# Kernel optimization log

Measured on AMD Instinct MI355X. Metric: run time of the kernel, lower is better.

## Reference

```python
import jax, jax.numpy as jnp
import numpy as np

SHORT_RANGE_CUTOFF = 1.6
N_PAIRS = 20_000_000
N_ATOMS = 100_000


def setup_inputs() -> dict:
    key = jax.random.key(0)
    k1, k2, k3 = jax.random.split(key, 3)
    Rij = jax.random.normal(k1, (N_PAIRS, 3), dtype=jnp.float32)
    idx_i = jax.random.randint(k2, (N_PAIRS,), 0, N_ATOMS, dtype=jnp.int64)
    idx_j = jax.random.randint(k3, (N_PAIRS,), 0, N_ATOMS, dtype=jnp.int64)
    return {"Rij": Rij, "idx_i": idx_i, "idx_j": idx_j}


def reference(Rij, idx_i, idx_j):
    """Faithful jax version of FilterShortRange.forward.

    torch.nonzero produces a dynamic-size index set; under jit we express the
    same compaction as a fixed-size stable partition: all pairs with
    ||Rij|| <= cutoff are packed to the front (original relative order
    preserved, matching torch.nonzero's ascending-index order), the tail is
    padded (Rij rows zeroed, idx entries set to -1), and n_valid reports the
    true compacted length.
    """
    rij = jnp.linalg.norm(Rij, axis=-1)                 # [P]
    mask = rij <= SHORT_RANGE_CUTOFF                    # [P] bool
    # stable argsort of ~mask: valid (False=0) entries first, order preserved
    order = jnp.argsort(jnp.logical_not(mask), stable=True)  # [P]
    mask_sorted = mask[order]                           # [P]
    Rij_sr = jnp.where(mask_sorted[:, None], Rij[order], 0.0)
    idx_i_sr = jnp.where(mask_sorted, idx_i[order], -1)
    idx_j_sr = jnp.where(mask_sorted, idx_j[order], -1)
    n_valid = jnp.sum(mask.astype(jnp.int32))
    # long-range copies are the untouched originals
    return (Rij_sr, idx_i_sr, idx_j_sr, Rij, idx_i, idx_j, n_valid)
```

## Files before the change

kernel.cpp:

```cpp
#include <hip/hip_runtime.h>
#include <math.h>


#define BLOCK 256
#define VPT 4
#define CHUNK (BLOCK * VPT)
#define SCAN_T 1024

__device__ __forceinline__ bool short_mask(float x, float y, float z) {
    float s = x * x + y * y + z * z;
    return sqrtf(s) <= 1.6f;
}

__global__ __launch_bounds__(BLOCK) void count_kernel(
    const float* __restrict__ Rij, int* __restrict__ counts, int P) {
    int b = blockIdx.x;
    int tid = threadIdx.x;
    int e0 = b * CHUNK + tid * VPT;
    int cnt = 0;
    if ((e0 + VPT <= P) && ((P & 3) == 0)) {
        const float4* R4 = (const float4*)Rij + (e0 * 3) / 4;
        float4 a = R4[0], c = R4[1], d = R4[2];
        cnt += short_mask(a.x, a.y, a.z);
        cnt += short_mask(a.w, c.x, c.y);
        cnt += short_mask(c.z, c.w, d.x);
        cnt += short_mask(d.y, d.z, d.w);
    } else {
        for (int j = 0; j < VPT; ++j) {
            int p = e0 + j;
            if (p < P) {
                float x = Rij[3 * p], y = Rij[3 * p + 1], z = Rij[3 * p + 2];
                cnt += short_mask(x, y, z);
            }
        }
    }
    for (int off = 32; off > 0; off >>= 1) cnt += __shfl_down(cnt, off);
    __shared__ int sm[BLOCK / 64];
    int lane = tid & 63, wid = tid >> 6;
    if (lane == 0) sm[wid] = cnt;
    __syncthreads();
    if (tid == 0) {
        int t = 0;
        for (int w = 0; w < BLOCK / 64; ++w) t += sm[w];
        counts[b] = t;
    }
}

__global__ __launch_bounds__(SCAN_T) void scan_kernel(
    const int* __restrict__ counts, int* __restrict__ offsets, int nb,
    int* __restrict__ nvalid_ws, float* __restrict__ nvalid_out) {
    __shared__ int sm[SCAN_T];
    __shared__ int carry_s;
    int tid = threadIdx.x;
    if (tid == 0) carry_s = 0;
    __syncthreads();
    for (int start = 0; start < nb; start += SCAN_T) {
        int i = start + tid;
        int v = (i < nb) ? counts[i] : 0;
        sm[tid] = v;
        __syncthreads();
        for (int off = 1; off < SCAN_T; off <<= 1) {
            int y = (tid >= off) ? sm[tid - off] : 0;
            __syncthreads();
            sm[tid] += y;
            __syncthreads();
        }
        int incl = sm[tid];
        int carry = carry_s;
        if (i < nb) offsets[i] = carry + incl - v;
        __syncthreads();
        if (tid == 0) carry_s = carry + sm[SCAN_T - 1];
        __syncthreads();
    }
    if (tid == 0) {
        nvalid_ws[0] = carry_s;
        nvalid_out[0] = (float)carry_s;
    }
}

__global__ __launch_bounds__(BLOCK) void scatter_kernel(
    const float* __restrict__ Rij, const int* __restrict__ idx_i,
    const int* __restrict__ idx_j, const int* __restrict__ offsets,
    const int* __restrict__ nvalid_ws, float* __restrict__ out, int P) {
    int b = blockIdx.x;
    int tid = threadIdx.x;
    int lane = tid & 63, wid = tid >> 6;
    int e0 = b * CHUNK + tid * VPT;
    int nvalid = nvalid_ws[0];

    float x[VPT], y[VPT], z[VPT];
    int ii[VPT], jj[VPT];
    bool m[VPT], inr[VPT];

    bool fullvec = (e0 + VPT <= P) && ((P & 3) == 0);
    if (fullvec) {
        const float4* R4 = (const float4*)Rij + (e0 * 3) / 4;
        float4 a = R4[0], c = R4[1], d = R4[2];
        x[0] = a.x; y[0] = a.y; z[0] = a.z;
        x[1] = a.w; y[1] = c.x; z[1] = c.y;
        x[2] = c.z; y[2] = c.w; z[2] = d.x;
        x[3] = d.y; y[3] = d.z; z[3] = d.w;
        int4 vi = *((const int4*)idx_i + e0 / 4);
        int4 vj = *((const int4*)idx_j + e0 / 4);
        ii[0] = vi.x; ii[1] = vi.y; ii[2] = vi.z; ii[3] = vi.w;
        jj[0] = vj.x; jj[1] = vj.y; jj[2] = vj.z; jj[3] = vj.w;
        for (int j = 0; j < VPT; ++j) {
            inr[j] = true;
            m[j] = short_mask(x[j], y[j], z[j]);
        }
        float4* lrR = (float4*)(out + 5LL * P) + (e0 * 3) / 4;
        lrR[0] = a; lrR[1] = c; lrR[2] = d;
        float4 fi = make_float4((float)ii[0], (float)ii[1], (float)ii[2], (float)ii[3]);
        float4 fj = make_float4((float)jj[0], (float)jj[1], (float)jj[2], (float)jj[3]);
        *((float4*)(out + 8LL * P) + e0 / 4) = fi;
        *((float4*)(out + 9LL * P) + e0 / 4) = fj;
    } else {
        for (int j = 0; j < VPT; ++j) {
            int p = e0 + j;
            inr[j] = (p < P);
            if (inr[j]) {
                x[j] = Rij[3 * p]; y[j] = Rij[3 * p + 1]; z[j] = Rij[3 * p + 2];
                ii[j] = idx_i[p]; jj[j] = idx_j[p];
                m[j] = short_mask(x[j], y[j], z[j]);
                out[5LL * P + 3 * p] = x[j];
                out[5LL * P + 3 * p + 1] = y[j];
                out[5LL * P + 3 * p + 2] = z[j];
                out[8LL * P + p] = (float)ii[j];
                out[9LL * P + p] = (float)jj[j];
            } else {
                m[j] = false;
            }
        }
    }

    int cnt = 0;
    for (int j = 0; j < VPT; ++j) cnt += (inr[j] && m[j]);

    int xs = cnt;
    for (int off = 1; off < 64; off <<= 1) {
        int yv = __shfl_up(xs, off);
        if (lane >= off) xs += yv;
    }
    int waveExcl = xs - cnt;
    __shared__ int wsum[BLOCK / 64];
    if (lane == 63) wsum[wid] = xs;
    __syncthreads();
    int wpre = 0;
    for (int w = 0; w < wid; ++w) wpre += wsum[w];

    int base = offsets[b] + wpre + waveExcl;
    int thrPre = 0;
    for (int j = 0; j < VPT; ++j) {
        if (!inr[j]) continue;
        int p = e0 + j;
        int v = base + thrPre;
        if (m[j]) {
            out[3 * v] = x[j];
            out[3 * v + 1] = y[j];
            out[3 * v + 2] = z[j];
            out[3LL * P + v] = (float)ii[j];
            out[4LL * P + v] = (float)jj[j];
            ++thrPre;
        } else {
            int dst = nvalid + (p - v);
            out[3 * dst] = 0.0f;
            out[3 * dst + 1] = 0.0f;
            out[3 * dst + 2] = 0.0f;
            out[3LL * P + dst] = -1.0f;
            out[4LL * P + dst] = -1.0f;
        }
    }
}

extern "C" void kernel_launch(void* const* d_in, const int* in_sizes, int n_in,
                              void* d_out, int out_size, void* d_ws, size_t ws_size,
                              hipStream_t stream) {
    const float* Rij = (const float*)d_in[0];
    const int* idx_i = (const int*)d_in[1];
    const int* idx_j = (const int*)d_in[2];
    int P = in_sizes[1];
    float* out = (float*)d_out;

    int nb = (P + CHUNK - 1) / CHUNK;
    int* counts = (int*)d_ws;
    int* offsets = counts + nb;
    int* nvalid_ws = offsets + nb;

    count_kernel<<<nb, BLOCK, 0, stream>>>(Rij, counts, P);
    scan_kernel<<<1, SCAN_T, 0, stream>>>(counts, offsets, nb, nvalid_ws,
                                          out + 10LL * P);
    scatter_kernel<<<nb, BLOCK, 0, stream>>>(Rij, idx_i, idx_j, offsets,
                                             nvalid_ws, out, P);
}
```

Baseline: 1.153 ms.

## Stage compacted pairs in LDS for coalesced writes, parallelize scan, use nontemporal stores

```diff
diff --git a/kernel.cpp b/kernel.cpp
--- a/kernel.cpp
+++ b/kernel.cpp
@@ -6,6 +6,9 @@
 #define VPT 4
 #define CHUNK (BLOCK * VPT)
 #define SCAN_T 1024
+
+typedef float vf4 __attribute__((ext_vector_type(4)));
+typedef int vi4 __attribute__((ext_vector_type(4)));
 
 __device__ __forceinline__ bool short_mask(float x, float y, float z) {
     float s = x * x + y * y + z * z;
@@ -18,9 +21,9 @@
     int tid = threadIdx.x;
     int e0 = b * CHUNK + tid * VPT;
     int cnt = 0;
-    if ((e0 + VPT <= P) && ((P & 3) == 0)) {
-        const float4* R4 = (const float4*)Rij + (e0 * 3) / 4;
-        float4 a = R4[0], c = R4[1], d = R4[2];
+    if (e0 + VPT <= P) {
+        const vf4* R4 = (const vf4*)Rij + (e0 * 3) / 4;
+        vf4 a = R4[0], c = R4[1], d = R4[2];
         cnt += short_mask(a.x, a.y, a.z);
         cnt += short_mask(a.w, c.x, c.y);
         cnt += short_mask(c.z, c.w, d.x);
@@ -49,32 +52,38 @@
 __global__ __launch_bounds__(SCAN_T) void scan_kernel(
     const int* __restrict__ counts, int* __restrict__ offsets, int nb,
     int* __restrict__ nvalid_ws, float* __restrict__ nvalid_out) {
-    __shared__ int sm[SCAN_T];
-    __shared__ int carry_s;
     int tid = threadIdx.x;
-    if (tid == 0) carry_s = 0;
-    __syncthreads();
-    for (int start = 0; start < nb; start += SCAN_T) {
-        int i = start + tid;
-        int v = (i < nb) ? counts[i] : 0;
-        sm[tid] = v;
-        __syncthreads();
-        for (int off = 1; off < SCAN_T; off <<= 1) {
-            int y = (tid >= off) ? sm[tid - off] : 0;
-            __syncthreads();
-            sm[tid] += y;
-            __syncthreads();
-        }
-        int incl = sm[tid];
-        int carry = carry_s;
-        if (i < nb) offsets[i] = carry + incl - v;
-        __syncthreads();
-        if (tid == 0) carry_s = carry + sm[SCAN_T - 1];
-        __syncthreads();
+    int seg = (nb + SCAN_T - 1) / SCAN_T;
+    int s0 = tid * seg;
+    int local = 0;
+    for (int k = 0; k < seg; ++k) {
+        int i = s0 + k;
+        if (i < nb) local += counts[i];
+    }
+    int lane = tid & 63, wid = tid >> 6;
+    int incl = local;
+    for (int off = 1; off < 64; off <<= 1) {
+        int y = __shfl_up(incl, off);
+        if (lane >= off) incl += y;
+    }
+    __shared__ int wsum[SCAN_T / 64];
+    if (lane == 63) wsum[wid] = incl;
+    __syncthreads();
+    int wpre = 0;
+    for (int w = 0; w < wid; ++w) wpre += wsum[w];
+    int run = wpre + incl - local;
+    for (int k = 0; k < seg; ++k) {
+        int i = s0 + k;
+        if (i < nb) {
+            offsets[i] = run;
+            run += counts[i];
+        }
     }
     if (tid == 0) {
-        nvalid_ws[0] = carry_s;
-        nvalid_out[0] = (float)carry_s;
+        int tot = 0;
+        for (int w = 0; w < SCAN_T / 64; ++w) tot += wsum[w];
+        nvalid_ws[0] = tot;
+        nvalid_out[0] = (float)tot;
     }
 }
 
@@ -82,43 +91,44 @@
     const float* __restrict__ Rij, const int* __restrict__ idx_i,
     const int* __restrict__ idx_j, const int* __restrict__ offsets,
     const int* __restrict__ nvalid_ws, float* __restrict__ out, int P) {
+    __shared__ float rs[3 * CHUNK];
+    __shared__ int iis[CHUNK];
+    __shared__ int jjs[CHUNK];
+    __shared__ int wsums[BLOCK / 64];
+
     int b = blockIdx.x;
     int tid = threadIdx.x;
     int lane = tid & 63, wid = tid >> 6;
     int e0 = b * CHUNK + tid * VPT;
-    int nvalid = nvalid_ws[0];
 
     float x[VPT], y[VPT], z[VPT];
     int ii[VPT], jj[VPT];
-    bool m[VPT], inr[VPT];
-
-    bool fullvec = (e0 + VPT <= P) && ((P & 3) == 0);
-    if (fullvec) {
-        const float4* R4 = (const float4*)Rij + (e0 * 3) / 4;
-        float4 a = R4[0], c = R4[1], d = R4[2];
+    bool m[VPT];
+
+    if (e0 + VPT <= P) {
+        const vf4* R4 = (const vf4*)Rij + (e0 * 3) / 4;
+        vf4 a = R4[0], c = R4[1], d = R4[2];
         x[0] = a.x; y[0] = a.y; z[0] = a.z;
         x[1] = a.w; y[1] = c.x; z[1] = c.y;
         x[2] = c.z; y[2] = c.w; z[2] = d.x;
         x[3] = d.y; y[3] = d.z; z[3] = d.w;
-        int4 vi = *((const int4*)idx_i + e0 / 4);
-        int4 vj = *((const int4*)idx_j + e0 / 4);
+        vi4 vi = *((const vi4*)idx_i + e0 / 4);
+        vi4 vj = *((const vi4*)idx_j + e0 / 4);
         ii[0] = vi.x; ii[1] = vi.y; ii[2] = vi.z; ii[3] = vi.w;
         jj[0] = vj.x; jj[1] = vj.y; jj[2] = vj.z; jj[3] = vj.w;
-        for (int j = 0; j < VPT; ++j) {
-            inr[j] = true;
-            m[j] = short_mask(x[j], y[j], z[j]);
-        }
-        float4* lrR = (float4*)(out + 5LL * P) + (e0 * 3) / 4;
-        lrR[0] = a; lrR[1] = c; lrR[2] = d;
-        float4 fi = make_float4((float)ii[0], (float)ii[1], (float)ii[2], (float)ii[3]);
-        float4 fj = make_float4((float)jj[0], (float)jj[1], (float)jj[2], (float)jj[3]);
-        *((float4*)(out + 8LL * P) + e0 / 4) = fi;
-        *((float4*)(out + 9LL * P) + e0 / 4) = fj;
+        for (int j = 0; j < VPT; ++j) m[j] = short_mask(x[j], y[j], z[j]);
+        vf4* lrR = (vf4*)(out + 5LL * P) + (e0 * 3) / 4;
+        __builtin_nontemporal_store(a, lrR + 0);
+        __builtin_nontemporal_store(c, lrR + 1);
+        __builtin_nontemporal_store(d, lrR + 2);
+        vf4 fi = {(float)ii[0], (float)ii[1], (float)ii[2], (float)ii[3]};
+        vf4 fj = {(float)jj[0], (float)jj[1], (float)jj[2], (float)jj[3]};
+        __builtin_nontemporal_store(fi, (vf4*)(out + 8LL * P) + e0 / 4);
+        __builtin_nontemporal_store(fj, (vf4*)(out + 9LL * P) + e0 / 4);
     } else {
         for (int j = 0; j < VPT; ++j) {
             int p = e0 + j;
-            inr[j] = (p < P);
-            if (inr[j]) {
+            if (p < P) {
                 x[j] = Rij[3 * p]; y[j] = Rij[3 * p + 1]; z[j] = Rij[3 * p + 2];
                 ii[j] = idx_i[p]; jj[j] = idx_j[p];
                 m[j] = short_mask(x[j], y[j], z[j]);
@@ -133,8 +143,7 @@
         }
     }
 
-    int cnt = 0;
-    for (int j = 0; j < VPT; ++j) cnt += (inr[j] && m[j]);
+    int cnt = (int)m[0] + (int)m[1] + (int)m[2] + (int)m[3];
 
     int xs = cnt;
     for (int off = 1; off < 64; off <<= 1) {
@@ -142,33 +151,44 @@
         if (lane >= off) xs += yv;
     }
     int waveExcl = xs - cnt;
-    __shared__ int wsum[BLOCK / 64];
-    if (lane == 63) wsum[wid] = xs;
+    if (lane == 63) wsums[wid] = xs;
     __syncthreads();
     int wpre = 0;
-    for (int w = 0; w < wid; ++w) wpre += wsum[w];
-
-    int base = offsets[b] + wpre + waveExcl;
-    int thrPre = 0;
+    for (int w = 0; w < wid; ++w) wpre += wsums[w];
+    int cntB = 0;
+    for (int w = 0; w < BLOCK / 64; ++w) cntB += wsums[w];
+
+    int lv = wpre + waveExcl;
     for (int j = 0; j < VPT; ++j) {
-        if (!inr[j]) continue;
-        int p = e0 + j;
-        int v = base + thrPre;
         if (m[j]) {
-            out[3 * v] = x[j];
-            out[3 * v + 1] = y[j];
-            out[3 * v + 2] = z[j];
-            out[3LL * P + v] = (float)ii[j];
-            out[4LL * P + v] = (float)jj[j];
-            ++thrPre;
-        } else {
-            int dst = nvalid + (p - v);
-            out[3 * dst] = 0.0f;
-            out[3 * dst + 1] = 0.0f;
-            out[3 * dst + 2] = 0.0f;
-            out[3LL * P + dst] = -1.0f;
-            out[4LL * P + dst] = -1.0f;
-        }
+            rs[3 * lv] = x[j];
+            rs[3 * lv + 1] = y[j];
+            rs[3 * lv + 2] = z[j];
+            iis[lv] = ii[j];
+            jjs[lv] = jj[j];
+            ++lv;
+        }
+    }
+    __syncthreads();
+
+    int gbase = offsets[b];
+    int nvalid = nvalid_ws[0];
+    int blockStart = b * CHUNK;
+    int blockN = min(CHUNK, P - blockStart);
+    int invB = blockN - cntB;
+    long long tailStart = (long long)nvalid + (blockStart - gbase);
+
+    for (int k = tid; k < 3 * cntB; k += BLOCK)
+        __builtin_nontemporal_store(rs[k], out + 3LL * gbase + k);
+    for (int k = tid; k < cntB; k += BLOCK) {
+        __builtin_nontemporal_store((float)iis[k], out + 3LL * P + gbase + k);
+        __builtin_nontemporal_store((float)jjs[k], out + 4LL * P + gbase + k);
+    }
+    for (int k = tid; k < 3 * invB; k += BLOCK)
+        __builtin_nontemporal_store(0.0f, out + 3LL * tailStart + k);
+    for (int k = tid; k < invB; k += BLOCK) {
+        __builtin_nontemporal_store(-1.0f, out + 3LL * P + tailStart + k);
+        __builtin_nontemporal_store(-1.0f, out + 4LL * P + tailStart + k);
     }
 }
 
```

After: 1.205 ms. 4.5% more time.
